# Kernel tuning notes

Measured on AMD Instinct MI355X. Metric: run time of the kernel, lower is better.

## Reference

```python
import jax, jax.numpy as jnp
import numpy as np

N = 50000      # nodes
E = 800000     # edges
G = 512        # graphs
H = 256        # hidden_dim
T = 32         # tag embedding dim
L = 4          # num_layers
EPS = 1e-5


def setup_inputs() -> dict:
    key = jax.random.key(0)
    ks = jax.random.split(key, 16)
    x = jax.random.randint(ks[0], (N,), 0, 100)
    tags = jax.random.randint(ks[1], (N,), 0, 3)
    edge_index = jax.random.randint(ks[2], (2, E), 0, N)
    batch = jnp.sort(jax.random.randint(ks[3], (N,), 0, G))
    s = 1.0 / np.sqrt(H)
    atom_emb = jax.random.normal(ks[4], (100, H), jnp.float32)
    tag_emb = jax.random.normal(ks[5], (3, T), jnp.float32)
    Wp = jax.random.normal(ks[6], (H + T, H), jnp.float32) * (1.0 / np.sqrt(H + T))
    bp = jnp.zeros((H,), jnp.float32)
    gcn_W = jax.random.normal(ks[7], (L, H, H), jnp.float32) * s
    gcn_b = jnp.zeros((L, H), jnp.float32)
    bn_g = jnp.ones((L, H), jnp.float32)
    bn_b = jnp.zeros((L, H), jnp.float32)
    W1 = jax.random.normal(ks[8], (H, H // 2), jnp.float32) * s
    b1 = jnp.zeros((H // 2,), jnp.float32)
    W2 = jax.random.normal(ks[9], (H // 2, 1), jnp.float32) * (1.0 / np.sqrt(H // 2))
    b2 = jnp.zeros((1,), jnp.float32)
    return dict(x=x, tags=tags, edge_index=edge_index, batch=batch,
                atom_emb=atom_emb, tag_emb=tag_emb, Wp=Wp, bp=bp,
                gcn_W=gcn_W, gcn_b=gcn_b, bn_g=bn_g, bn_b=bn_b,
                W1=W1, b1=b1, W2=W2, b2=b2)


def _gcn_conv(h, W, b, src, dst, dinv):
    # PyG GCNConv: x' = W x, symmetric normalization with self-loops.
    hw = h @ W                                   # [N, H]
    norm = dinv[src] * dinv[dst]                 # [E]
    msg = hw[src] * norm[:, None]                # [E, H]  (gather)
    agg = jax.ops.segment_sum(msg, dst, num_segments=N)  # scatter-add
    agg = agg + hw * (dinv * dinv)[:, None]      # self-loop term
    return agg + b


def _batch_norm(x, g, b):
    mu = jnp.mean(x, axis=0)
    var = jnp.var(x, axis=0)
    return (x - mu) * jax.lax.rsqrt(var + EPS) * g + b


def reference(x, tags, edge_index, batch, atom_emb, tag_emb, Wp, bp,
              gcn_W, gcn_b, bn_g, bn_b, W1, b1, W2, b2):
    src, dst = edge_index[0], edge_index[1]
    # degree with self-loops (gcn_norm counts on the dst/col index)
    deg = jax.ops.segment_sum(jnp.ones((E,), jnp.float32), dst, num_segments=N) + 1.0
    dinv = jax.lax.rsqrt(deg)

    h = jnp.concatenate([atom_emb[x], tag_emb[tags]], axis=1) @ Wp + bp  # [N, H]
    for l in range(L):
        res = h
        h = _gcn_conv(h, gcn_W[l], gcn_b[l], src, dst, dinv)
        h = jax.nn.relu(_batch_norm(h, bn_g[l], bn_b[l]))
        h = h + res                                  # dropout is identity in eval

    # global mean pool over graphs
    sums = jax.ops.segment_sum(h, batch, num_segments=G)
    cnts = jax.ops.segment_sum(jnp.ones((N,), jnp.float32), batch, num_segments=G)
    pooled = sums / jnp.maximum(cnts, 1.0)[:, None]  # [G, H]

    hid = jax.nn.relu(pooled @ W1 + b1)
    energy = hid @ W2 + b2                           # [G, 1]
    return energy.squeeze(-1)
```

## Files before the change

### kernel.cpp

```cpp
#include <hip/hip_runtime.h>
#include <hip/hip_bf16.h>

#define NN 50000
#define EE 800000
#define GG 512
#define HH 256
#define TT 32
#define LL 4
#define EPSF 1e-5f

typedef __attribute__((ext_vector_type(8))) short short8;
typedef __attribute__((ext_vector_type(4))) float float4v;

__device__ inline unsigned short f2b(float f) {
    unsigned u = __float_as_uint(f);
    unsigned r = (u + 0x7FFFu + ((u >> 16) & 1u)) >> 16;
    return (unsigned short)r;
}
__device__ inline float4 bf4_to_f4(ushort4 u) {
    float4 f;
    f.x = __uint_as_float((unsigned)u.x << 16);
    f.y = __uint_as_float((unsigned)u.y << 16);
    f.z = __uint_as_float((unsigned)u.z << 16);
    f.w = __uint_as_float((unsigned)u.w << 16);
    return f;
}

__global__ void k_degree(const int* __restrict__ dst, int* __restrict__ cnt, int E) {
    int e = blockIdx.x * 256 + threadIdx.x;
    if (e < E) atomicAdd(&cnt[dst[e]], 1);
}

__global__ void k_dinv(const int* __restrict__ cnt, float* __restrict__ dinv, int N) {
    int i = blockIdx.x * 256 + threadIdx.x;
    if (i < N) dinv[i] = rsqrtf((float)cnt[i] + 1.0f);
}

__global__ void k_scan1(const int* __restrict__ cnt, int* __restrict__ incl,
                        int* __restrict__ bsum, int N) {
    __shared__ int s[1024];
    int i = blockIdx.x * 1024 + threadIdx.x;
    int v = (i < N) ? cnt[i] : 0;
    s[threadIdx.x] = v;
    __syncthreads();
    for (int off = 1; off < 1024; off <<= 1) {
        int t = (threadIdx.x >= off) ? s[threadIdx.x - off] : 0;
        __syncthreads();
        s[threadIdx.x] += t;
        __syncthreads();
    }
    if (i < N) incl[i] = s[threadIdx.x];
    if (threadIdx.x == 1023) bsum[blockIdx.x] = s[1023];
}

__global__ void k_scan2(int* __restrict__ bsum, int nb) {
    __shared__ int s[64];
    int v = (threadIdx.x < nb) ? bsum[threadIdx.x] : 0;
    s[threadIdx.x] = v;
    __syncthreads();
    for (int off = 1; off < 64; off <<= 1) {
        int t = (threadIdx.x >= off) ? s[threadIdx.x - off] : 0;
        __syncthreads();
        s[threadIdx.x] += t;
        __syncthreads();
    }
    if (threadIdx.x < nb) bsum[threadIdx.x] = s[threadIdx.x] - v;
}

__global__ void k_scan3(int* __restrict__ rs, const int* __restrict__ cnt,
                        const int* __restrict__ boff, int N) {
    int i = blockIdx.x * 256 + threadIdx.x;
    if (i < N) rs[i] = rs[i] + boff[i >> 10] - cnt[i];
}

__global__ void k_scatter(const int* __restrict__ src, const int* __restrict__ dst,
                          const int* __restrict__ rs, int* __restrict__ cur,
                          int* __restrict__ csr, int E) {
    int e = blockIdx.x * 256 + threadIdx.x;
    if (e >= E) return;
    int d = dst[e];
    int p = rs[d] + atomicAdd(&cur[d], 1);
    csr[p] = src[e];
}

__global__ void k_wprep(const float* __restrict__ W, unsigned short* __restrict__ Wt) {
    int l = blockIdx.y;
    int n = blockIdx.x * 4 + (threadIdx.x >> 6);
    int kq = (threadIdx.x & 63) * 4;
    const float* Wl = W + (size_t)l * HH * HH;
    ushort4 o;
    o.x = f2b(Wl[(size_t)(kq + 0) * HH + n]);
    o.y = f2b(Wl[(size_t)(kq + 1) * HH + n]);
    o.z = f2b(Wl[(size_t)(kq + 2) * HH + n]);
    o.w = f2b(Wl[(size_t)(kq + 3) * HH + n]);
    *(ushort4*)(Wt + (size_t)l * HH * HH + (size_t)n * HH + kq) = o;
}

__global__ void k_proj(const float* __restrict__ atom_emb, const float* __restrict__ tag_emb,
                       const float* __restrict__ Wp, const float* __restrict__ bp,
                       float* __restrict__ aref, float* __restrict__ tref) {
    int r = blockIdx.x;
    int j = threadIdx.x;
    if (r < 100) {
        float acc = bp[j];
        for (int k = 0; k < HH; ++k) acc += atom_emb[r * HH + k] * Wp[(size_t)k * HH + j];
        aref[r * HH + j] = acc;
    } else {
        int tr = r - 100;
        float acc = 0.f;
        for (int k = 0; k < TT; ++k) acc += tag_emb[tr * TT + k] * Wp[(size_t)(HH + k) * HH + j];
        tref[tr * HH + j] = acc;
    }
}

__global__ void k_h0(const int* __restrict__ x, const int* __restrict__ tags,
                     const float* __restrict__ aref, const float* __restrict__ tref,
                     unsigned short* __restrict__ hb, int N) {
    int n = blockIdx.x;
    int lane = threadIdx.x;
    float4 a = ((const float4*)(aref + (size_t)x[n] * HH))[lane];
    float4 t = ((const float4*)(tref + (size_t)tags[n] * HH))[lane];
    ushort4 u;
    u.x = f2b(a.x + t.x); u.y = f2b(a.y + t.y);
    u.z = f2b(a.z + t.z); u.w = f2b(a.w + t.w);
    ((ushort4*)(hb + (size_t)n * HH))[lane] = u;
}

__global__ __launch_bounds__(256) void k_gemm(const unsigned short* __restrict__ hb,
                                              const unsigned short* __restrict__ Wt,
                                              const float* __restrict__ dinv,
                                              unsigned short* __restrict__ hwb, int M) {
    __shared__ unsigned short As[128][72];
    __shared__ unsigned short Bs[128][72];
    int t = threadIdx.x;
    int lane = t & 63, w = t >> 6;
    int wr = w >> 1, wc = w & 1;
    int l15 = lane & 15, l4 = lane >> 4;
    int row0 = blockIdx.y * 128, col0 = blockIdx.x * 128;
    float4v acc[4][4];
#pragma unroll
    for (int i = 0; i < 4; ++i)
#pragma unroll
        for (int j = 0; j < 4; ++j) acc[i][j] = (float4v)0.f;

    for (int k0 = 0; k0 < 256; k0 += 64) {
        if (k0) __syncthreads();
#pragma unroll
        for (int u = 0; u < 4; ++u) {
            int idx = u * 256 + t;
            int r = idx >> 3;
            int c = (idx & 7) * 8;
            *(uint4*)&As[r][c] = *(const uint4*)(hb + (size_t)(row0 + r) * 256 + k0 + c);
            *(uint4*)&Bs[r][c] = *(const uint4*)(Wt + (size_t)(col0 + r) * 256 + k0 + c);
        }
        __syncthreads();
#pragma unroll
        for (int kk = 0; kk < 64; kk += 32) {
            short8 a[4], b[4];
#pragma unroll
            for (int i = 0; i < 4; ++i)
                a[i] = *(const short8*)&As[wr * 64 + i * 16 + l15][kk + l4 * 8];
#pragma unroll
            for (int i = 0; i < 4; ++i)
                b[i] = *(const short8*)&Bs[wc * 64 + i * 16 + l15][kk + l4 * 8];
#pragma unroll
            for (int mi = 0; mi < 4; ++mi)
#pragma unroll
                for (int ni = 0; ni < 4; ++ni)
                    acc[mi][ni] = __builtin_amdgcn_mfma_f32_16x16x32_bf16(
                        a[mi], b[ni], acc[mi][ni], 0, 0, 0);
        }
    }
#pragma unroll
    for (int mi = 0; mi < 4; ++mi) {
        int mb = row0 + wr * 64 + mi * 16 + l4 * 4;
        float dv[4];
#pragma unroll
        for (int r = 0; r < 4; ++r) dv[r] = (mb + r < M) ? dinv[mb + r] : 0.f;
#pragma unroll
        for (int ni = 0; ni < 4; ++ni) {
            int n = col0 + wc * 64 + ni * 16 + l15;
#pragma unroll
            for (int r = 0; r < 4; ++r) {
                if (mb + r < M)
                    hwb[(size_t)(mb + r) * 256 + n] = f2b(acc[mi][ni][r] * dv[r]);
            }
        }
    }
}

__global__ void k_agg(const unsigned short* __restrict__ hwb, float* __restrict__ agg,
                      const int* __restrict__ csr, const int* __restrict__ rs,
                      const int* __restrict__ cnt, const float* __restrict__ dinv,
                      const float* __restrict__ bias, int N) {
    int wave = threadIdx.x >> 6;
    int lane = threadIdx.x & 63;
    int n = blockIdx.x * 4 + wave;
    if (n >= N) return;
    float dn = dinv[n];
    int e = rs[n];
    int end = e + cnt[n];
    float4 acc = bf4_to_f4(((const ushort4*)(hwb + (size_t)n * HH))[lane]);
    for (; e + 8 <= end; e += 8) {
        int s0 = csr[e],     s1 = csr[e + 1], s2 = csr[e + 2], s3 = csr[e + 3];
        int s4 = csr[e + 4], s5 = csr[e + 5], s6 = csr[e + 6], s7 = csr[e + 7];
        float4 m0 = bf4_to_f4(((const ushort4*)(hwb + (size_t)s0 * HH))[lane]);
        float4 m1 = bf4_to_f4(((const ushort4*)(hwb + (size_t)s1 * HH))[lane]);
        float4 m2 = bf4_to_f4(((const ushort4*)(hwb + (size_t)s2 * HH))[lane]);
        float4 m3 = bf4_to_f4(((const ushort4*)(hwb + (size_t)s3 * HH))[lane]);
        float4 m4 = bf4_to_f4(((const ushort4*)(hwb + (size_t)s4 * HH))[lane]);
        float4 m5 = bf4_to_f4(((const ushort4*)(hwb + (size_t)s5 * HH))[lane]);
        float4 m6 = bf4_to_f4(((const ushort4*)(hwb + (size_t)s6 * HH))[lane]);
        float4 m7 = bf4_to_f4(((const ushort4*)(hwb + (size_t)s7 * HH))[lane]);
        acc.x += ((m0.x + m1.x) + (m2.x + m3.x)) + ((m4.x + m5.x) + (m6.x + m7.x));
        acc.y += ((m0.y + m1.y) + (m2.y + m3.y)) + ((m4.y + m5.y) + (m6.y + m7.y));
        acc.z += ((m0.z + m1.z) + (m2.z + m3.z)) + ((m4.z + m5.z) + (m6.z + m7.z));
        acc.w += ((m0.w + m1.w) + (m2.w + m3.w)) + ((m4.w + m5.w) + (m6.w + m7.w));
    }
    for (; e + 4 <= end; e += 4) {
        int s0 = csr[e], s1 = csr[e + 1], s2 = csr[e + 2], s3 = csr[e + 3];
        float4 m0 = bf4_to_f4(((const ushort4*)(hwb + (size_t)s0 * HH))[lane]);
        float4 m1 = bf4_to_f4(((const ushort4*)(hwb + (size_t)s1 * HH))[lane]);
        float4 m2 = bf4_to_f4(((const ushort4*)(hwb + (size_t)s2 * HH))[lane]);
        float4 m3 = bf4_to_f4(((const ushort4*)(hwb + (size_t)s3 * HH))[lane]);
        acc.x += (m0.x + m1.x) + (m2.x + m3.x);
        acc.y += (m0.y + m1.y) + (m2.y + m3.y);
        acc.z += (m0.z + m1.z) + (m2.z + m3.z);
        acc.w += (m0.w + m1.w) + (m2.w + m3.w);
    }
    for (; e < end; ++e) {
        int s = csr[e];
        float4 m = bf4_to_f4(((const ushort4*)(hwb + (size_t)s * HH))[lane]);
        acc.x += m.x; acc.y += m.y; acc.z += m.z; acc.w += m.w;
    }
    float4 b = ((const float4*)bias)[lane];
    float4 r;
    r.x = acc.x * dn + b.x; r.y = acc.y * dn + b.y;
    r.z = acc.z * dn + b.z; r.w = acc.w * dn + b.w;
    ((float4*)(agg + (size_t)n * HH))[lane] = r;
}

__global__ __launch_bounds__(256) void k_bnstats(const float4* __restrict__ agg,
                                                 float* __restrict__ colsum,
                                                 float* __restrict__ colsq, int N) {
    __shared__ float4 ssum[4][64];
    __shared__ float4 ssq[4][64];
    int lane = threadIdx.x & 63;
    int wv = threadIdx.x >> 6;
    int rows_per = (N + gridDim.x - 1) / gridDim.x;
    int r0 = blockIdx.x * rows_per;
    int r1 = r0 + rows_per; if (r1 > N) r1 = N;
    float4 s = make_float4(0.f, 0.f, 0.f, 0.f);
    float4 s2 = make_float4(0.f, 0.f, 0.f, 0.f);
    for (int r = r0 + wv; r < r1; r += 4) {
        float4 v = agg[(size_t)r * 64 + lane];
        s.x += v.x; s.y += v.y; s.z += v.z; s.w += v.w;
        s2.x += v.x * v.x; s2.y += v.y * v.y; s2.z += v.z * v.z; s2.w += v.w * v.w;
    }
    ssum[wv][lane] = s;
    ssq[wv][lane] = s2;
    __syncthreads();
    int j = lane * 4;
    if (wv == 0) {
        float4 a = ssum[0][lane], b = ssum[1][lane], c = ssum[2][lane], d = ssum[3][lane];
        atomicAdd(&colsum[j + 0], a.x + b.x + c.x + d.x);
        atomicAdd(&colsum[j + 1], a.y + b.y + c.y + d.y);
        atomicAdd(&colsum[j + 2], a.z + b.z + c.z + d.z);
        atomicAdd(&colsum[j + 3], a.w + b.w + c.w + d.w);
    } else if (wv == 1) {
        float4 a = ssq[0][lane], b = ssq[1][lane], c = ssq[2][lane], d = ssq[3][lane];
        atomicAdd(&colsq[j + 0], a.x + b.x + c.x + d.x);
        atomicAdd(&colsq[j + 1], a.y + b.y + c.y + d.y);
        atomicAdd(&colsq[j + 2], a.z + b.z + c.z + d.z);
        atomicAdd(&colsq[j + 3], a.w + b.w + c.w + d.w);
    }
}

__global__ void k_epi(const float4* __restrict__ agg, ushort4* __restrict__ hb,
                      const float4* __restrict__ colsum, const float4* __restrict__ colsq,
                      const float4* __restrict__ g4, const float4* __restrict__ b4,
                      int total, float invN) {
    int idx = blockIdx.x * 256 + threadIdx.x;
    if (idx >= total) return;
    int q = idx & 63;
    float4 a = agg[idx];
    float4 s = colsum[q], s2 = colsq[q], g = g4[q], b = b4[q];
    float4 hv = bf4_to_f4(hb[idx]);
    float mu, var, v;
    mu = s.x * invN; var = s2.x * invN - mu * mu;
    v = (a.x - mu) * rsqrtf(var + EPSF) * g.x + b.x; hv.x += fmaxf(v, 0.f);
    mu = s.y * invN; var = s2.y * invN - mu * mu;
    v = (a.y - mu) * rsqrtf(var + EPSF) * g.y + b.y; hv.y += fmaxf(v, 0.f);
    mu = s.z * invN; var = s2.z * invN - mu * mu;
    v = (a.z - mu) * rsqrtf(var + EPSF) * g.z + b.z; hv.z += fmaxf(v, 0.f);
    mu = s.w * invN; var = s2.w * invN - mu * mu;
    v = (a.w - mu) * rsqrtf(var + EPSF) * g.w + b.w; hv.w += fmaxf(v, 0.f);
    ushort4 u;
    u.x = f2b(hv.x); u.y = f2b(hv.y); u.z = f2b(hv.z); u.w = f2b(hv.w);
    hb[idx] = u;
}

__global__ void k_ginit(int* __restrict__ gstart, int G, int N) {
    int g = blockIdx.x * 256 + threadIdx.x;
    if (g <= G) gstart[g] = N;
}

__global__ void k_gbound(const int* __restrict__ batch, int* __restrict__ gstart, int N) {
    int n = blockIdx.x * 256 + threadIdx.x;
    if (n >= N) return;
    int b = batch[n];
    int prev = (n == 0) ? -1 : batch[n - 1];
    for (int g = prev + 1; g <= b; ++g) gstart[g] = n;
}

__global__ void k_pool(const unsigned short* __restrict__ hb, const int* __restrict__ gstart,
                       float* __restrict__ pooled) {
    __shared__ float4 sm[4][64];
    int g = blockIdx.x;
    int t = threadIdx.x;
    int lane = t & 63, wv = t >> 6;
    int s = gstart[g], e = gstart[g + 1];
    float4 acc = make_float4(0.f, 0.f, 0.f, 0.f);
    for (int n = s + wv; n < e; n += 4) {
        float4 v = bf4_to_f4(((const ushort4*)(hb + (size_t)n * HH))[lane]);
        acc.x += v.x; acc.y += v.y; acc.z += v.z; acc.w += v.w;
    }
    sm[wv][lane] = acc;
    __syncthreads();
    if (wv == 0) {
        float4 a = sm[0][lane], b = sm[1][lane], c = sm[2][lane], d = sm[3][lane];
        float inv = 1.0f / fmaxf((float)(e - s), 1.0f);
        float4 r;
        r.x = (a.x + b.x + c.x + d.x) * inv;
        r.y = (a.y + b.y + c.y + d.y) * inv;
        r.z = (a.z + b.z + c.z + d.z) * inv;
        r.w = (a.w + b.w + c.w + d.w) * inv;
        ((float4*)pooled)[(size_t)g * 64 + lane] = r;
    }
}

__global__ void k_head(const float* __restrict__ pooled,
                       const float* __restrict__ W1, const float* __restrict__ b1,
                       const float* __restrict__ W2, const float* __restrict__ b2,
                       float* __restrict__ out) {
    __shared__ float prow[256];
    __shared__ float hred[128];
    int g = blockIdx.x, t = threadIdx.x;
    prow[t] = pooled[(size_t)g * HH + t];
    prow[t + 128] = pooled[(size_t)g * HH + t + 128];
    __syncthreads();
    float acc = b1[t];
    for (int k = 0; k < HH; ++k) acc += prow[k] * W1[(size_t)k * 128 + t];
    float hid = fmaxf(acc, 0.f);
    hred[t] = hid * W2[t];
    __syncthreads();
    for (int off = 64; off > 0; off >>= 1) {
        if (t < off) hred[t] += hred[t + off];
        __syncthreads();
    }
    if (t == 0) out[g] = hred[0] + b2[0];
}

extern "C" void kernel_launch(void* const* d_in, const int* in_sizes, int n_in,
                              void* d_out, int out_size, void* d_ws, size_t ws_size,
                              hipStream_t stream) {
    const int* x        = (const int*)d_in[0];
    const int* tags     = (const int*)d_in[1];
    const int* ei       = (const int*)d_in[2];
    const int* batch    = (const int*)d_in[3];
    const float* atom_e = (const float*)d_in[4];
    const float* tag_e  = (const float*)d_in[5];
    const float* Wp     = (const float*)d_in[6];
    const float* bp     = (const float*)d_in[7];
    const float* gcn_W  = (const float*)d_in[8];
    const float* gcn_b  = (const float*)d_in[9];
    const float* bn_g   = (const float*)d_in[10];
    const float* bn_b   = (const float*)d_in[11];
    const float* W1     = (const float*)d_in[12];
    const float* b1     = (const float*)d_in[13];
    const float* W2     = (const float*)d_in[14];
    const float* b2     = (const float*)d_in[15];
    float* out = (float*)d_out;

    const int N = NN, E = EE, G = GG, H = HH;
    const int Mpad = ((N + 127) / 128) * 128;

    char* p = (char*)d_ws;
    auto alloc = [&](size_t bytes) {
        void* r = (void*)p;
        p += (bytes + 255) & ~(size_t)255;
        return r;
    };
    unsigned short* hb  = (unsigned short*)alloc((size_t)Mpad * H * 2);
    unsigned short* hwb = (unsigned short*)alloc((size_t)Mpad * H * 2);
    unsigned short* Wt  = (unsigned short*)alloc((size_t)LL * H * H * 2);
    float* agg  = (float*)alloc((size_t)N * H * 4);
    float* dinv = (float*)alloc((size_t)N * 4);
    int* cnt    = (int*)alloc((size_t)N * 4);
    int* rs     = (int*)alloc((size_t)N * 4);
    int* cur    = (int*)alloc((size_t)N * 4);
    int* csr    = (int*)alloc((size_t)E * 4);
    int* bsum   = (int*)alloc(64 * 4);
    float* aref = (float*)alloc(100 * (size_t)H * 4);
    float* tref = (float*)alloc(3 * (size_t)H * 4);
    float* cstat= (float*)alloc(2 * (size_t)H * 4);
    int* gstart = (int*)alloc((size_t)(G + 1) * 4);
    float* pooled = (float*)alloc((size_t)G * H * 4);

    const int* src = ei;
    const int* dst = ei + E;

    hipMemsetAsync(cnt, 0, (size_t)N * 4, stream);
    hipMemsetAsync(cur, 0, (size_t)N * 4, stream);

    k_degree<<<(E + 255) / 256, 256, 0, stream>>>(dst, cnt, E);
    k_dinv<<<(N + 255) / 256, 256, 0, stream>>>(cnt, dinv, N);

    int nb = (N + 1023) / 1024;
    k_scan1<<<nb, 1024, 0, stream>>>(cnt, rs, bsum, N);
    k_scan2<<<1, 64, 0, stream>>>(bsum, nb);
    k_scan3<<<(N + 255) / 256, 256, 0, stream>>>(rs, cnt, bsum, N);
    k_scatter<<<(E + 255) / 256, 256, 0, stream>>>(src, dst, rs, cur, csr, E);

    k_ginit<<<(G + 256) / 256, 256, 0, stream>>>(gstart, G, N);
    k_gbound<<<(N + 255) / 256, 256, 0, stream>>>(batch, gstart, N);

    k_wprep<<<dim3(64, LL), 256, 0, stream>>>(gcn_W, Wt);
    k_proj<<<103, 256, 0, stream>>>(atom_e, tag_e, Wp, bp, aref, tref);
    k_h0<<<N, 64, 0, stream>>>(x, tags, aref, tref, hb, N);

    for (int l = 0; l < LL; ++l) {
        k_gemm<<<dim3(2, Mpad / 128), 256, 0, stream>>>(
            hb, Wt + (size_t)l * H * H, dinv, hwb, N);
        k_agg<<<(N + 3) / 4, 256, 0, stream>>>(hwb, agg, csr, rs, cnt, dinv,
                                               gcn_b + (size_t)l * H, N);
        hipMemsetAsync(cstat, 0, 2 * (size_t)H * 4, stream);
        k_bnstats<<<512, 256, 0, stream>>>((const float4*)agg, cstat, cstat + H, N);
        k_epi<<<(N * 64 + 255) / 256, 256, 0, stream>>>(
            (const float4*)agg, (ushort4*)hb,
            (const float4*)cstat, (const float4*)(cstat + H),
            (const float4*)(bn_g + (size_t)l * H), (const float4*)(bn_b + (size_t)l * H),
            N * 64, 1.0f / (float)N);
    }

    k_pool<<<G, 256, 0, stream>>>(hb, gstart, pooled);
    k_head<<<G, 128, 0, stream>>>(pooled, W1, b1, W2, b2, out);
}
```

Baseline: 899.9 us.

## Store GEMM output column-chunked and split aggregation by feature chunk, bf16 agg

The GEMM now writes hw in 8 column chunks of 32 features each (chunk-major, row stride 32), so each chunk is a compact 3.2MB table that fits in cache. The aggregation kernel launches one grid slice per chunk, and each wave gathers four neighbours at once with 16 lanes per neighbour, then reduces with shuffles. The self-loop is folded into the neighbour list as item 0. The aggregation output is stored as bf16 instead of fp32, which halves the traffic for the BN stats and epilogue kernels. The cost is more index loads (8x re-reading the CSR), strided GEMM stores, and an extra rounding to bf16 before batch norm.

```diff
diff --git a/kernel.cpp b/kernel.cpp
--- a/kernel.cpp
+++ b/kernel.cpp
@@ -129,7 +129,8 @@
 __global__ __launch_bounds__(256) void k_gemm(const unsigned short* __restrict__ hb,
                                               const unsigned short* __restrict__ Wt,
                                               const float* __restrict__ dinv,
-                                              unsigned short* __restrict__ hwb, int M) {
+                                              unsigned short* __restrict__ hwc,
+                                              int M, int Mpad) {
     __shared__ unsigned short As[128][72];
     __shared__ unsigned short Bs[128][72];
     int t = threadIdx.x;
@@ -180,67 +181,72 @@
 #pragma unroll
         for (int ni = 0; ni < 4; ++ni) {
             int n = col0 + wc * 64 + ni * 16 + l15;
+            int ch = n >> 5, wi = n & 31;
+            unsigned short* obase = hwc + (size_t)ch * Mpad * 32 + wi;
 #pragma unroll
             for (int r = 0; r < 4; ++r) {
                 if (mb + r < M)
-                    hwb[(size_t)(mb + r) * 256 + n] = f2b(acc[mi][ni][r] * dv[r]);
+                    obase[(size_t)(mb + r) * 32] = f2b(acc[mi][ni][r] * dv[r]);
             }
         }
     }
 }
 
-__global__ void k_agg(const unsigned short* __restrict__ hwb, float* __restrict__ agg,
+__global__ __launch_bounds__(256) void k_agg(const unsigned short* __restrict__ hwc,
+                      unsigned short* __restrict__ aggb,
                       const int* __restrict__ csr, const int* __restrict__ rs,
                       const int* __restrict__ cnt, const float* __restrict__ dinv,
-                      const float* __restrict__ bias, int N) {
+                      const float* __restrict__ bias, int N, int Mpad) {
     int wave = threadIdx.x >> 6;
     int lane = threadIdx.x & 63;
     int n = blockIdx.x * 4 + wave;
     if (n >= N) return;
+    int c = blockIdx.y;
+    const unsigned short* base = hwc + (size_t)c * Mpad * 32;
+    int q = lane >> 4;
+    int colp = lane & 15;
     float dn = dinv[n];
-    int e = rs[n];
-    int end = e + cnt[n];
-    float4 acc = bf4_to_f4(((const ushort4*)(hwb + (size_t)n * HH))[lane]);
-    for (; e + 8 <= end; e += 8) {
-        int s0 = csr[e],     s1 = csr[e + 1], s2 = csr[e + 2], s3 = csr[e + 3];
-        int s4 = csr[e + 4], s5 = csr[e + 5], s6 = csr[e + 6], s7 = csr[e + 7];
-        float4 m0 = bf4_to_f4(((const ushort4*)(hwb + (size_t)s0 * HH))[lane]);
-        float4 m1 = bf4_to_f4(((const ushort4*)(hwb + (size_t)s1 * HH))[lane]);
-        float4 m2 = bf4_to_f4(((const ushort4*)(hwb + (size_t)s2 * HH))[lane]);
-        float4 m3 = bf4_to_f4(((const ushort4*)(hwb + (size_t)s3 * HH))[lane]);
-        float4 m4 = bf4_to_f4(((const ushort4*)(hwb + (size_t)s4 * HH))[lane]);
-        float4 m5 = bf4_to_f4(((const ushort4*)(hwb + (size_t)s5 * HH))[lane]);
-        float4 m6 = bf4_to_f4(((const ushort4*)(hwb + (size_t)s6 * HH))[lane]);
-        float4 m7 = bf4_to_f4(((const ushort4*)(hwb + (size_t)s7 * HH))[lane]);
-        acc.x += ((m0.x + m1.x) + (m2.x + m3.x)) + ((m4.x + m5.x) + (m6.x + m7.x));
-        acc.y += ((m0.y + m1.y) + (m2.y + m3.y)) + ((m4.y + m5.y) + (m6.y + m7.y));
-        acc.z += ((m0.z + m1.z) + (m2.z + m3.z)) + ((m4.z + m5.z) + (m6.z + m7.z));
-        acc.w += ((m0.w + m1.w) + (m2.w + m3.w)) + ((m4.w + m5.w) + (m6.w + m7.w));
-    }
-    for (; e + 4 <= end; e += 4) {
-        int s0 = csr[e], s1 = csr[e + 1], s2 = csr[e + 2], s3 = csr[e + 3];
-        float4 m0 = bf4_to_f4(((const ushort4*)(hwb + (size_t)s0 * HH))[lane]);
-        float4 m1 = bf4_to_f4(((const ushort4*)(hwb + (size_t)s1 * HH))[lane]);
-        float4 m2 = bf4_to_f4(((const ushort4*)(hwb + (size_t)s2 * HH))[lane]);
-        float4 m3 = bf4_to_f4(((const ushort4*)(hwb + (size_t)s3 * HH))[lane]);
-        acc.x += (m0.x + m1.x) + (m2.x + m3.x);
-        acc.y += (m0.y + m1.y) + (m2.y + m3.y);
-        acc.z += (m0.z + m1.z) + (m2.z + m3.z);
-        acc.w += (m0.w + m1.w) + (m2.w + m3.w);
-    }
-    for (; e < end; ++e) {
-        int s = csr[e];
-        float4 m = bf4_to_f4(((const ushort4*)(hwb + (size_t)s * HH))[lane]);
-        acc.x += m.x; acc.y += m.y; acc.z += m.z; acc.w += m.w;
-    }
-    float4 b = ((const float4*)bias)[lane];
-    float4 r;
-    r.x = acc.x * dn + b.x; r.y = acc.y * dn + b.y;
-    r.z = acc.z * dn + b.z; r.w = acc.w * dn + b.w;
-    ((float4*)(agg + (size_t)n * HH))[lane] = r;
-}
-
-__global__ __launch_bounds__(256) void k_bnstats(const float4* __restrict__ agg,
+    int start = rs[n] - 1;
+    int len = cnt[n] + 1;
+    float accx = 0.f, accy = 0.f;
+    int i = 0;
+    for (; i + 16 <= len; i += 16) {
+        int i0 = i + q;
+        int r0 = (i0 == 0) ? n : csr[start + i0];
+        int r1 = csr[start + i0 + 4];
+        int r2 = csr[start + i0 + 8];
+        int r3 = csr[start + i0 + 12];
+        unsigned v0 = *(const unsigned*)(base + (size_t)r0 * 32 + colp * 2);
+        unsigned v1 = *(const unsigned*)(base + (size_t)r1 * 32 + colp * 2);
+        unsigned v2 = *(const unsigned*)(base + (size_t)r2 * 32 + colp * 2);
+        unsigned v3 = *(const unsigned*)(base + (size_t)r3 * 32 + colp * 2);
+        accx += (__uint_as_float(v0 << 16) + __uint_as_float(v1 << 16))
+              + (__uint_as_float(v2 << 16) + __uint_as_float(v3 << 16));
+        accy += (__uint_as_float(v0 & 0xFFFF0000u) + __uint_as_float(v1 & 0xFFFF0000u))
+              + (__uint_as_float(v2 & 0xFFFF0000u) + __uint_as_float(v3 & 0xFFFF0000u));
+    }
+    for (; i < len; i += 4) {
+        int item = i + q;
+        if (item < len) {
+            int row = (item == 0) ? n : csr[start + item];
+            unsigned v = *(const unsigned*)(base + (size_t)row * 32 + colp * 2);
+            accx += __uint_as_float(v << 16);
+            accy += __uint_as_float(v & 0xFFFF0000u);
+        }
+    }
+    accx += __shfl_xor(accx, 16);
+    accy += __shfl_xor(accy, 16);
+    accx += __shfl_xor(accx, 32);
+    accy += __shfl_xor(accy, 32);
+    if (q == 0) {
+        int col = c * 32 + colp * 2;
+        unsigned short ux = f2b(accx * dn + bias[col]);
+        unsigned short uy = f2b(accy * dn + bias[col + 1]);
+        *(unsigned*)(aggb + (size_t)n * 256 + col) = (unsigned)ux | ((unsigned)uy << 16);
+    }
+}
+
+__global__ __launch_bounds__(256) void k_bnstats(const ushort4* __restrict__ aggb,
                                                  float* __restrict__ colsum,
                                                  float* __restrict__ colsq, int N) {
     __shared__ float4 ssum[4][64];
@@ -253,7 +259,7 @@
     float4 s = make_float4(0.f, 0.f, 0.f, 0.f);
     float4 s2 = make_float4(0.f, 0.f, 0.f, 0.f);
     for (int r = r0 + wv; r < r1; r += 4) {
-        float4 v = agg[(size_t)r * 64 + lane];
+        float4 v = bf4_to_f4(aggb[(size_t)r * 64 + lane]);
         s.x += v.x; s.y += v.y; s.z += v.z; s.w += v.w;
         s2.x += v.x * v.x; s2.y += v.y * v.y; s2.z += v.z * v.z; s2.w += v.w * v.w;
     }
@@ -276,14 +282,14 @@
     }
 }
 
-__global__ void k_epi(const float4* __restrict__ agg, ushort4* __restrict__ hb,
+__global__ void k_epi(const ushort4* __restrict__ aggb, ushort4* __restrict__ hb,
                       const float4* __restrict__ colsum, const float4* __restrict__ colsq,
                       const float4* __restrict__ g4, const float4* __restrict__ b4,
                       int total, float invN) {
     int idx = blockIdx.x * 256 + threadIdx.x;
     if (idx >= total) return;
     int q = idx & 63;
-    float4 a = agg[idx];
+    float4 a = bf4_to_f4(aggb[idx]);
     float4 s = colsum[q], s2 = colsq[q], g = g4[q], b = b4[q];
     float4 hv = bf4_to_f4(hb[idx]);
     float mu, var, v;
@@ -392,9 +398,9 @@
         return r;
     };
     unsigned short* hb  = (unsigned short*)alloc((size_t)Mpad * H * 2);
-    unsigned short* hwb = (unsigned short*)alloc((size_t)Mpad * H * 2);
+    unsigned short* hwc = (unsigned short*)alloc((size_t)Mpad * H * 2);
     unsigned short* Wt  = (unsigned short*)alloc((size_t)LL * H * H * 2);
-    float* agg  = (float*)alloc((size_t)N * H * 4);
+    unsigned short* aggb= (unsigned short*)alloc((size_t)N * H * 2);
     float* dinv = (float*)alloc((size_t)N * 4);
     int* cnt    = (int*)alloc((size_t)N * 4);
     int* rs     = (int*)alloc((size_t)N * 4);
@@ -431,13 +437,13 @@
 
     for (int l = 0; l < LL; ++l) {
         k_gemm<<<dim3(2, Mpad / 128), 256, 0, stream>>>(
-            hb, Wt + (size_t)l * H * H, dinv, hwb, N);
-        k_agg<<<(N + 3) / 4, 256, 0, stream>>>(hwb, agg, csr, rs, cnt, dinv,
-                                               gcn_b + (size_t)l * H, N);
+            hb, Wt + (size_t)l * H * H, dinv, hwc, N, Mpad);
+        k_agg<<<dim3((N + 3) / 4, 8), 256, 0, stream>>>(hwc, aggb, csr, rs, cnt, dinv,
+                                                        gcn_b + (size_t)l * H, N, Mpad);
         hipMemsetAsync(cstat, 0, 2 * (size_t)H * 4, stream);
-        k_bnstats<<<512, 256, 0, stream>>>((const float4*)agg, cstat, cstat + H, N);
+        k_bnstats<<<512, 256, 0, stream>>>((const ushort4*)aggb, cstat, cstat + H, N);
         k_epi<<<(N * 64 + 255) / 256, 256, 0, stream>>>(
-            (const float4*)agg, (ushort4*)hb,
+            (const ushort4*)aggb, (ushort4*)hb,
             (const float4*)cstat, (const float4*)(cstat + H),
             (const float4*)(bn_g + (size_t)l * H), (const float4*)(bn_b + (size_t)l * H),
             N * 64, 1.0f / (float)N);
```

New measurement: 1.304 ms. 1.45x slower.

## Fuse BN/ReLU/residual epilogue into next GEMM prologue, store aggregate in bf16

Applied to the files above, without the earlier changes.

The separate per-layer epilogue kernel is removed. The next layer's GEMM now applies batch-norm, ReLU and the residual while loading its A tile, and writes the updated h to a ping-pong buffer. The first layer builds h0 from the embedding tables inside the GEMM, and the final layer's epilogue is folded into pooling. The aggregate buffer is stored in bf16 instead of fp32, and small setup kernels and memsets are merged. Together these cut HBM traffic and launch count, at the cost of extra precision loss in the aggregate and redundant epilogue work across the two column blocks.

```diff
diff --git a/kernel.cpp b/kernel.cpp
--- a/kernel.cpp
+++ b/kernel.cpp
@@ -17,6 +17,9 @@
     unsigned r = (u + 0x7FFFu + ((u >> 16) & 1u)) >> 16;
     return (unsigned short)r;
 }
+__device__ inline unsigned pack2(float lo, float hi) {
+    return (unsigned)f2b(lo) | ((unsigned)f2b(hi) << 16);
+}
 __device__ inline float4 bf4_to_f4(ushort4 u) {
     float4 f;
     f.x = __uint_as_float((unsigned)u.x << 16);
@@ -31,11 +34,6 @@
     if (e < E) atomicAdd(&cnt[dst[e]], 1);
 }
 
-__global__ void k_dinv(const int* __restrict__ cnt, float* __restrict__ dinv, int N) {
-    int i = blockIdx.x * 256 + threadIdx.x;
-    if (i < N) dinv[i] = rsqrtf((float)cnt[i] + 1.0f);
-}
-
 __global__ void k_scan1(const int* __restrict__ cnt, int* __restrict__ incl,
                         int* __restrict__ bsum, int N) {
     __shared__ int s[1024];
@@ -68,9 +66,13 @@
 }
 
 __global__ void k_scan3(int* __restrict__ rs, const int* __restrict__ cnt,
-                        const int* __restrict__ boff, int N) {
+                        const int* __restrict__ boff, float* __restrict__ dinv, int N) {
     int i = blockIdx.x * 256 + threadIdx.x;
-    if (i < N) rs[i] = rs[i] + boff[i >> 10] - cnt[i];
+    if (i < N) {
+        int c = cnt[i];
+        rs[i] = rs[i] + boff[i >> 10] - c;
+        dinv[i] = rsqrtf((float)c + 1.0f);
+    }
 }
 
 __global__ void k_scatter(const int* __restrict__ src, const int* __restrict__ dst,
@@ -83,60 +85,83 @@
     csr[p] = src[e];
 }
 
-__global__ void k_wprep(const float* __restrict__ W, unsigned short* __restrict__ Wt) {
-    int l = blockIdx.y;
-    int n = blockIdx.x * 4 + (threadIdx.x >> 6);
-    int kq = (threadIdx.x & 63) * 4;
-    const float* Wl = W + (size_t)l * HH * HH;
-    ushort4 o;
-    o.x = f2b(Wl[(size_t)(kq + 0) * HH + n]);
-    o.y = f2b(Wl[(size_t)(kq + 1) * HH + n]);
-    o.z = f2b(Wl[(size_t)(kq + 2) * HH + n]);
-    o.w = f2b(Wl[(size_t)(kq + 3) * HH + n]);
-    *(ushort4*)(Wt + (size_t)l * HH * HH + (size_t)n * HH + kq) = o;
-}
-
-__global__ void k_proj(const float* __restrict__ atom_emb, const float* __restrict__ tag_emb,
-                       const float* __restrict__ Wp, const float* __restrict__ bp,
-                       float* __restrict__ aref, float* __restrict__ tref) {
-    int r = blockIdx.x;
-    int j = threadIdx.x;
-    if (r < 100) {
-        float acc = bp[j];
-        for (int k = 0; k < HH; ++k) acc += atom_emb[r * HH + k] * Wp[(size_t)k * HH + j];
-        aref[r * HH + j] = acc;
+__global__ void k_gbound(const int* __restrict__ batch, int* __restrict__ gstart,
+                         int N, int G) {
+    int n = blockIdx.x * 256 + threadIdx.x;
+    if (n >= N) return;
+    int b = batch[n];
+    int prev = (n == 0) ? -1 : batch[n - 1];
+    for (int g = prev + 1; g <= b; ++g) gstart[g] = n;
+    if (n == N - 1)
+        for (int g = b + 1; g <= G; ++g) gstart[g] = N;
+}
+
+__global__ void k_projw(const float* __restrict__ atom_emb, const float* __restrict__ tag_emb,
+                        const float* __restrict__ Wp, const float* __restrict__ bp,
+                        const float* __restrict__ W,
+                        float* __restrict__ aref, float* __restrict__ tref,
+                        unsigned short* __restrict__ Wt) {
+    int blk = blockIdx.x;
+    if (blk < 256) {
+        int l = blk >> 6;
+        int bx = blk & 63;
+        int n = bx * 4 + (threadIdx.x >> 6);
+        int kq = (threadIdx.x & 63) * 4;
+        const float* Wl = W + (size_t)l * HH * HH;
+        ushort4 o;
+        o.x = f2b(Wl[(size_t)(kq + 0) * HH + n]);
+        o.y = f2b(Wl[(size_t)(kq + 1) * HH + n]);
+        o.z = f2b(Wl[(size_t)(kq + 2) * HH + n]);
+        o.w = f2b(Wl[(size_t)(kq + 3) * HH + n]);
+        *(ushort4*)(Wt + (size_t)l * HH * HH + (size_t)n * HH + kq) = o;
     } else {
-        int tr = r - 100;
-        float acc = 0.f;
-        for (int k = 0; k < TT; ++k) acc += tag_emb[tr * TT + k] * Wp[(size_t)(HH + k) * HH + j];
-        tref[tr * HH + j] = acc;
-    }
-}
-
-__global__ void k_h0(const int* __restrict__ x, const int* __restrict__ tags,
-                     const float* __restrict__ aref, const float* __restrict__ tref,
-                     unsigned short* __restrict__ hb, int N) {
-    int n = blockIdx.x;
-    int lane = threadIdx.x;
-    float4 a = ((const float4*)(aref + (size_t)x[n] * HH))[lane];
-    float4 t = ((const float4*)(tref + (size_t)tags[n] * HH))[lane];
-    ushort4 u;
-    u.x = f2b(a.x + t.x); u.y = f2b(a.y + t.y);
-    u.z = f2b(a.z + t.z); u.w = f2b(a.w + t.w);
-    ((ushort4*)(hb + (size_t)n * HH))[lane] = u;
-}
-
-__global__ __launch_bounds__(256) void k_gemm(const unsigned short* __restrict__ hb,
-                                              const unsigned short* __restrict__ Wt,
-                                              const float* __restrict__ dinv,
-                                              unsigned short* __restrict__ hwb, int M) {
+        int r = blk - 256;
+        int j = threadIdx.x;
+        if (r < 100) {
+            float acc = bp[j];
+            for (int k = 0; k < HH; ++k) acc += atom_emb[r * HH + k] * Wp[(size_t)k * HH + j];
+            aref[r * HH + j] = acc;
+        } else {
+            int tr = r - 100;
+            float acc = 0.f;
+            for (int k = 0; k < TT; ++k) acc += tag_emb[tr * TT + k] * Wp[(size_t)(HH + k) * HH + j];
+            tref[tr * HH + j] = acc;
+        }
+    }
+}
+
+__global__ __launch_bounds__(256) void k_gemm(
+    const unsigned short* __restrict__ hb_read,
+    const unsigned short* __restrict__ Wt,
+    const float* __restrict__ dinv,
+    unsigned short* __restrict__ hwb,
+    int mode,
+    const int* __restrict__ x, const int* __restrict__ tags,
+    const float* __restrict__ aref, const float* __restrict__ tref,
+    const unsigned short* __restrict__ aggb,
+    const float* __restrict__ colsum, const float* __restrict__ colsq,
+    const float* __restrict__ bng, const float* __restrict__ bnb,
+    unsigned short* __restrict__ hb_out,
+    int M, float invN) {
     __shared__ unsigned short As[128][72];
     __shared__ unsigned short Bs[128][72];
+    __shared__ float sc[256], sh[256];
     int t = threadIdx.x;
     int lane = t & 63, w = t >> 6;
     int wr = w >> 1, wc = w & 1;
     int l15 = lane & 15, l4 = lane >> 4;
     int row0 = blockIdx.y * 128, col0 = blockIdx.x * 128;
+    bool wantWrite = (blockIdx.x == 0);
+
+    if (mode == 1) {
+        float mu = colsum[t] * invN;
+        float var = colsq[t] * invN - mu * mu;
+        float s = bng[t] * rsqrtf(var + EPSF);
+        sc[t] = s;
+        sh[t] = bnb[t] - mu * s;
+    }
+    __syncthreads();
+
     float4v acc[4][4];
 #pragma unroll
     for (int i = 0; i < 4; ++i)
@@ -150,8 +175,45 @@
             int idx = u * 256 + t;
             int r = idx >> 3;
             int c = (idx & 7) * 8;
-            *(uint4*)&As[r][c] = *(const uint4*)(hb + (size_t)(row0 + r) * 256 + k0 + c);
-            *(uint4*)&Bs[r][c] = *(const uint4*)(Wt + (size_t)(col0 + r) * 256 + k0 + c);
+            int grow = row0 + r;
+            int gcol = k0 + c;
+            *(uint4*)&Bs[r][c] = *(const uint4*)(Wt + (size_t)(col0 + r) * 256 + gcol);
+            uint4 ov;
+            if (grow < M) {
+                unsigned o[4];
+                if (mode == 0) {
+                    const float* ar = aref + (size_t)x[grow] * 256 + gcol;
+                    const float* tr = tref + (size_t)tags[grow] * 256 + gcol;
+                    float4 a0 = *(const float4*)ar, a1 = *(const float4*)(ar + 4);
+                    float4 t0 = *(const float4*)tr, t1 = *(const float4*)(tr + 4);
+                    o[0] = pack2(a0.x + t0.x, a0.y + t0.y);
+                    o[1] = pack2(a0.z + t0.z, a0.w + t0.w);
+                    o[2] = pack2(a1.x + t1.x, a1.y + t1.y);
+                    o[3] = pack2(a1.z + t1.z, a1.w + t1.w);
+                } else {
+                    uint4 hv = *(const uint4*)(hb_read + (size_t)grow * 256 + gcol);
+                    uint4 av = *(const uint4*)(aggb + (size_t)grow * 256 + gcol);
+                    const unsigned* hvp = (const unsigned*)&hv;
+                    const unsigned* avp = (const unsigned*)&av;
+#pragma unroll
+                    for (int j = 0; j < 4; ++j) {
+                        unsigned hj = hvp[j], aj = avp[j];
+                        float h0 = __uint_as_float(hj << 16);
+                        float h1 = __uint_as_float(hj & 0xFFFF0000u);
+                        float a0 = __uint_as_float(aj << 16);
+                        float a1 = __uint_as_float(aj & 0xFFFF0000u);
+                        int cc = gcol + j * 2;
+                        float v0 = fmaxf(a0 * sc[cc] + sh[cc], 0.f);
+                        float v1 = fmaxf(a1 * sc[cc + 1] + sh[cc + 1], 0.f);
+                        o[j] = pack2(h0 + v0, h1 + v1);
+                    }
+                }
+                ov = make_uint4(o[0], o[1], o[2], o[3]);
+                if (wantWrite) *(uint4*)(hb_out + (size_t)grow * 256 + gcol) = ov;
+            } else {
+                ov = make_uint4(0u, 0u, 0u, 0u);
+            }
+            *(uint4*)&As[r][c] = ov;
         }
         __syncthreads();
 #pragma unroll
@@ -189,7 +251,7 @@
     }
 }
 
-__global__ void k_agg(const unsigned short* __restrict__ hwb, float* __restrict__ agg,
+__global__ void k_agg(const unsigned short* __restrict__ hwb, unsigned short* __restrict__ aggb,
                       const int* __restrict__ csr, const int* __restrict__ rs,
                       const int* __restrict__ cnt, const float* __restrict__ dinv,
                       const float* __restrict__ bias, int N) {
@@ -234,13 +296,13 @@
         acc.x += m.x; acc.y += m.y; acc.z += m.z; acc.w += m.w;
     }
     float4 b = ((const float4*)bias)[lane];
-    float4 r;
-    r.x = acc.x * dn + b.x; r.y = acc.y * dn + b.y;
-    r.z = acc.z * dn + b.z; r.w = acc.w * dn + b.w;
-    ((float4*)(agg + (size_t)n * HH))[lane] = r;
-}
-
-__global__ __launch_bounds__(256) void k_bnstats(const float4* __restrict__ agg,
+    ushort4 u;
+    u.x = f2b(acc.x * dn + b.x); u.y = f2b(acc.y * dn + b.y);
+    u.z = f2b(acc.z * dn + b.z); u.w = f2b(acc.w * dn + b.w);
+    ((ushort4*)(aggb + (size_t)n * HH))[lane] = u;
+}
+
+__global__ __launch_bounds__(256) void k_bnstats(const ushort4* __restrict__ aggb,
                                                  float* __restrict__ colsum,
                                                  float* __restrict__ colsq, int N) {
     __shared__ float4 ssum[4][64];
@@ -253,7 +315,7 @@
     float4 s = make_float4(0.f, 0.f, 0.f, 0.f);
     float4 s2 = make_float4(0.f, 0.f, 0.f, 0.f);
     for (int r = r0 + wv; r < r1; r += 4) {
-        float4 v = agg[(size_t)r * 64 + lane];
+        float4 v = bf4_to_f4(aggb[(size_t)r * 64 + lane]);
         s.x += v.x; s.y += v.y; s.z += v.z; s.w += v.w;
         s2.x += v.x * v.x; s2.y += v.y * v.y; s2.z += v.z * v.z; s2.w += v.w * v.w;
     }
@@ -276,54 +338,36 @@
     }
 }
 
-__global__ void k_epi(const float4* __restrict__ agg, ushort4* __restrict__ hb,
-                      const float4* __restrict__ colsum, const float4* __restrict__ colsq,
-                      const float4* __restrict__ g4, const float4* __restrict__ b4,
-                      int total, float invN) {
-    int idx = blockIdx.x * 256 + threadIdx.x;
-    if (idx >= total) return;
-    int q = idx & 63;
-    float4 a = agg[idx];
-    float4 s = colsum[q], s2 = colsq[q], g = g4[q], b = b4[q];
-    float4 hv = bf4_to_f4(hb[idx]);
-    float mu, var, v;
-    mu = s.x * invN; var = s2.x * invN - mu * mu;
-    v = (a.x - mu) * rsqrtf(var + EPSF) * g.x + b.x; hv.x += fmaxf(v, 0.f);
-    mu = s.y * invN; var = s2.y * invN - mu * mu;
-    v = (a.y - mu) * rsqrtf(var + EPSF) * g.y + b.y; hv.y += fmaxf(v, 0.f);
-    mu = s.z * invN; var = s2.z * invN - mu * mu;
-    v = (a.z - mu) * rsqrtf(var + EPSF) * g.z + b.z; hv.z += fmaxf(v, 0.f);
-    mu = s.w * invN; var = s2.w * invN - mu * mu;
-    v = (a.w - mu) * rsqrtf(var + EPSF) * g.w + b.w; hv.w += fmaxf(v, 0.f);
-    ushort4 u;
-    u.x = f2b(hv.x); u.y = f2b(hv.y); u.z = f2b(hv.z); u.w = f2b(hv.w);
-    hb[idx] = u;
-}
-
-__global__ void k_ginit(int* __restrict__ gstart, int G, int N) {
-    int g = blockIdx.x * 256 + threadIdx.x;
-    if (g <= G) gstart[g] = N;
-}
-
-__global__ void k_gbound(const int* __restrict__ batch, int* __restrict__ gstart, int N) {
-    int n = blockIdx.x * 256 + threadIdx.x;
-    if (n >= N) return;
-    int b = batch[n];
-    int prev = (n == 0) ? -1 : batch[n - 1];
-    for (int g = prev + 1; g <= b; ++g) gstart[g] = n;
-}
-
-__global__ void k_pool(const unsigned short* __restrict__ hb, const int* __restrict__ gstart,
-                       float* __restrict__ pooled) {
+__global__ void k_pool(const unsigned short* __restrict__ hb,
+                       const unsigned short* __restrict__ aggb,
+                       const int* __restrict__ gstart,
+                       const float* __restrict__ colsum, const float* __restrict__ colsq,
+                       const float* __restrict__ bng, const float* __restrict__ bnb,
+                       float* __restrict__ pooled, float invN) {
     __shared__ float4 sm[4][64];
     int g = blockIdx.x;
     int t = threadIdx.x;
     int lane = t & 63, wv = t >> 6;
+    int col = lane * 4;
+    float4 cs = *(const float4*)(colsum + col);
+    float4 cq = *(const float4*)(colsq + col);
+    float4 gg = *(const float4*)(bng + col);
+    float4 bb = *(const float4*)(bnb + col);
+    float4 scl, shf;
+    float mu, var;
+    mu = cs.x * invN; var = cq.x * invN - mu * mu; scl.x = gg.x * rsqrtf(var + EPSF); shf.x = bb.x - mu * scl.x;
+    mu = cs.y * invN; var = cq.y * invN - mu * mu; scl.y = gg.y * rsqrtf(var + EPSF); shf.y = bb.y - mu * scl.y;
+    mu = cs.z * invN; var = cq.z * invN - mu * mu; scl.z = gg.z * rsqrtf(var + EPSF); shf.z = bb.z - mu * scl.z;
+    mu = cs.w * invN; var = cq.w * invN - mu * mu; scl.w = gg.w * rsqrtf(var + EPSF); shf.w = bb.w - mu * scl.w;
     int s = gstart[g], e = gstart[g + 1];
     float4 acc = make_float4(0.f, 0.f, 0.f, 0.f);
     for (int n = s + wv; n < e; n += 4) {
-        float4 v = bf4_to_f4(((const ushort4*)(hb + (size_t)n * HH))[lane]);
-        acc.x += v.x; acc.y += v.y; acc.z += v.z; acc.w += v.w;
+        float4 hv = bf4_to_f4(((const ushort4*)(hb + (size_t)n * HH))[lane]);
+        float4 av = bf4_to_f4(((const ushort4*)(aggb + (size_t)n * HH))[lane]);
+        acc.x += hv.x + fmaxf(av.x * scl.x + shf.x, 0.f);
+        acc.y += hv.y + fmaxf(av.y * scl.y + shf.y, 0.f);
+        acc.z += hv.z + fmaxf(av.z * scl.z + shf.z, 0.f);
+        acc.w += hv.w + fmaxf(av.w * scl.w + shf.w, 0.f);
     }
     sm[wv][lane] = acc;
     __syncthreads();
@@ -384,6 +428,7 @@
 
     const int N = NN, E = EE, G = GG, H = HH;
     const int Mpad = ((N + 127) / 128) * 128;
+    const float invN = 1.0f / (float)N;
 
     char* p = (char*)d_ws;
     auto alloc = [&](size_t bytes) {
@@ -391,58 +436,58 @@
         p += (bytes + 255) & ~(size_t)255;
         return r;
     };
-    unsigned short* hb  = (unsigned short*)alloc((size_t)Mpad * H * 2);
+    unsigned short* hbA = (unsigned short*)alloc((size_t)Mpad * H * 2);
+    unsigned short* hbB = (unsigned short*)alloc((size_t)Mpad * H * 2);
     unsigned short* hwb = (unsigned short*)alloc((size_t)Mpad * H * 2);
     unsigned short* Wt  = (unsigned short*)alloc((size_t)LL * H * H * 2);
-    float* agg  = (float*)alloc((size_t)N * H * 4);
+    unsigned short* aggb= (unsigned short*)alloc((size_t)N * H * 2);
     float* dinv = (float*)alloc((size_t)N * 4);
-    int* cnt    = (int*)alloc((size_t)N * 4);
     int* rs     = (int*)alloc((size_t)N * 4);
-    int* cur    = (int*)alloc((size_t)N * 4);
     int* csr    = (int*)alloc((size_t)E * 4);
     int* bsum   = (int*)alloc(64 * 4);
     float* aref = (float*)alloc(100 * (size_t)H * 4);
     float* tref = (float*)alloc(3 * (size_t)H * 4);
-    float* cstat= (float*)alloc(2 * (size_t)H * 4);
     int* gstart = (int*)alloc((size_t)(G + 1) * 4);
     float* pooled = (float*)alloc((size_t)G * H * 4);
+    int* cnt    = (int*)alloc((size_t)N * 4);
+    int* cur    = (int*)alloc((size_t)N * 4);
+    float* cstat= (float*)alloc((size_t)LL * 512 * 4);
+    size_t zspan = (size_t)((char*)cstat + (size_t)LL * 512 * 4 - (char*)cnt);
 
     const int* src = ei;
     const int* dst = ei + E;
 
-    hipMemsetAsync(cnt, 0, (size_t)N * 4, stream);
-    hipMemsetAsync(cur, 0, (size_t)N * 4, stream);
+    hipMemsetAsync(cnt, 0, zspan, stream);
 
     k_degree<<<(E + 255) / 256, 256, 0, stream>>>(dst, cnt, E);
-    k_dinv<<<(N + 255) / 256, 256, 0, stream>>>(cnt, dinv, N);
-
     int nb = (N + 1023) / 1024;
     k_scan1<<<nb, 1024, 0, stream>>>(cnt, rs, bsum, N);
     k_scan2<<<1, 64, 0, stream>>>(bsum, nb);
-    k_scan3<<<(N + 255) / 256, 256, 0, stream>>>(rs, cnt, bsum, N);
+    k_scan3<<<(N + 255) / 256, 256, 0, stream>>>(rs, cnt, bsum, dinv, N);
     k_scatter<<<(E + 255) / 256, 256, 0, stream>>>(src, dst, rs, cur, csr, E);
-
-    k_ginit<<<(G + 256) / 256, 256, 0, stream>>>(gstart, G, N);
-    k_gbound<<<(N + 255) / 256, 256, 0, stream>>>(batch, gstart, N);
-
-    k_wprep<<<dim3(64, LL), 256, 0, stream>>>(gcn_W, Wt);
-    k_proj<<<103, 256, 0, stream>>>(atom_e, tag_e, Wp, bp, aref, tref);
-    k_h0<<<N, 64, 0, stream>>>(x, tags, aref, tref, hb, N);
-
+    k_gbound<<<(N + 255) / 256, 256, 0, stream>>>(batch, gstart, N, G);
+    k_projw<<<359, 256, 0, stream>>>(atom_e, tag_e, Wp, bp, gcn_W, aref, tref, Wt);
+
+    unsigned short* hbw[4] = {hbA, hbB, hbA, hbB};
     for (int l = 0; l < LL; ++l) {
+        const unsigned short* hr = (l == 0) ? hbA : hbw[l - 1];
+        const float* cprev = cstat + (size_t)(l > 0 ? l - 1 : 0) * 512;
+        const float* bngp = bn_g + (size_t)(l > 0 ? l - 1 : 0) * H;
+        const float* bnbp = bn_b + (size_t)(l > 0 ? l - 1 : 0) * H;
         k_gemm<<<dim3(2, Mpad / 128), 256, 0, stream>>>(
-            hb, Wt + (size_t)l * H * H, dinv, hwb, N);
-        k_agg<<<(N + 3) / 4, 256, 0, stream>>>(hwb, agg, csr, rs, cnt, dinv,
+            hr, Wt + (size_t)l * H * H, dinv, hwb,
+            (l == 0) ? 0 : 1, x, tags, aref, tref, aggb,
+            cprev, cprev + 256, bngp, bnbp, hbw[l], N, invN);
+        k_agg<<<(N + 3) / 4, 256, 0, stream>>>(hwb, aggb, csr, rs, cnt, dinv,
                                                gcn_b + (size_t)l * H, N);
-        hipMemsetAsync(cstat, 0, 2 * (size_t)H * 4, stream);
-        k_bnstats<<<512, 256, 0, stream>>>((const float4*)agg, cstat, cstat + H, N);
-        k_epi<<<(N * 64 + 255) / 256, 256, 0, stream>>>(
-            (const float4*)agg, (ushort4*)hb,
-            (const float4*)cstat, (const float4*)(cstat + H),
-            (const float4*)(bn_g + (size_t)l * H), (const float4*)(bn_b + (size_t)l * H),
-            N * 64, 1.0f / (float)N);
-    }
-
-    k_pool<<<G, 256, 0, stream>>>(hb, gstart, pooled);
+        k_bnstats<<<512, 256, 0, stream>>>((const ushort4*)aggb,
+                                           cstat + (size_t)l * 512,
+                                           cstat + (size_t)l * 512 + 256, N);
+    }
+
+    k_pool<<<G, 256, 0, stream>>>(hbw[3], aggb, gstart,
+                                  cstat + 3 * 512, cstat + 3 * 512 + 256,
+                                  bn_g + 3 * (size_t)H, bn_b + 3 * (size_t)H,
+                                  pooled, invN);
     k_head<<<G, 128, 0, stream>>>(pooled, W1, b1, W2, b2, out);
 }
```

Result: faster. 866.8 us (-3.7%).
